# Kernel tuning notes

Hardware: AMD Instinct MI355X
Metric: run time of the kernel (lower is better)

The kernel has to match this reference:

```python
import jax, jax.numpy as jnp
import numpy as np

SPATIAL_SCALE = 0.0625
GAMMA = 0.1  # mmcv DeformRoIPool default
NUM_HEADS = 1


def deform_roi_pool(features, rois, offsets, spatial_scale=SPATIAL_SCALE, gamma=GAMMA):
    """mmcv-style deformable RoI (align) pooling, sampling_ratio=1.
    features: (B,C,H,W); rois: (N,5)=[b,x1,y1,x2,y2]; offsets: (P,oh,ow,2) (dw,dh).
    Returns (P,N,C,oh,ow)."""
    B, C, H, W = features.shape
    N = rois.shape[0]
    P, oh, ow, _ = offsets.shape
    bidx = rois[:, 0].astype(jnp.int32)
    x1 = rois[:, 1] * spatial_scale - 0.5
    y1 = rois[:, 2] * spatial_scale - 0.5
    rw = rois[:, 3] * spatial_scale - 0.5 - x1
    rh = rois[:, 4] * spatial_scale - 0.5 - y1
    bin_w = rw / ow
    bin_h = rh / oh
    gh = jnp.arange(oh, dtype=features.dtype)
    gw = jnp.arange(ow, dtype=features.dtype)
    # bin-center sample points (sampling_ratio=1), deformed by gamma*roi_size*offset
    y = (y1[:, None, None] + (gh[None, :, None] + 0.5) * bin_h[:, None, None])[None]
    y = y + gamma * rh[None, :, None, None] * offsets[:, None, :, :, 1]  # (P,N,oh,ow)
    x = (x1[:, None, None] + (gw[None, None, :] + 0.5) * bin_w[:, None, None])[None]
    x = x + gamma * rw[None, :, None, None] * offsets[:, None, :, :, 0]
    valid = (y > -1.0) & (y < H) & (x > -1.0) & (x < W)
    yc = jnp.clip(y, 0.0, H - 1)
    xc = jnp.clip(x, 0.0, W - 1)
    y0 = jnp.floor(yc).astype(jnp.int32)
    x0 = jnp.floor(xc).astype(jnp.int32)
    y1i = jnp.minimum(y0 + 1, H - 1)
    x1i = jnp.minimum(x0 + 1, W - 1)
    ly = yc - y0.astype(yc.dtype)
    lx = xc - x0.astype(xc.dtype)
    hy = 1.0 - ly
    hx = 1.0 - lx
    f = features.reshape(B, C, H * W)
    bb = jnp.broadcast_to(bidx[None, :, None, None], (P, N, oh, ow))

    def g(yi, xi):
        return f[bb, :, yi * W + xi]  # (P,N,oh,ow,C)

    val = (g(y0, x0) * (hy * hx)[..., None] + g(y0, x1i) * (hy * lx)[..., None]
           + g(y1i, x0) * (ly * hx)[..., None] + g(y1i, x1i) * (ly * lx)[..., None])
    val = jnp.where(valid[..., None], val, 0.0)
    return jnp.transpose(val, (0, 1, 4, 2, 3))  # (P,N,C,oh,ow)


def setup_inputs() -> dict:
    key = jax.random.key(0)
    ks = jax.random.split(key, 9)
    B, C, Hf, Wf = 4, 256, 128, 128
    N, oh, ow, P = 512, 7, 7, 4
    features = jax.random.normal(ks[0], (B, C, Hf, Wf), jnp.float32)
    bidx = jax.random.randint(ks[1], (N,), 0, B).astype(jnp.float32)
    xy1 = jax.random.uniform(ks[2], (N, 2), jnp.float32, 0.0, 1700.0)
    wh = jax.random.uniform(ks[3], (N, 2), jnp.float32, 32.0, 300.0)
    rois = jnp.concatenate([bidx[:, None], xy1, xy1 + wh], axis=1)  # (N,5)
    per_point_offsets = jax.random.normal(ks[4], (P, oh, ow, 2), jnp.float32) * 0.001
    queries = jax.random.normal(ks[5], (oh * ow, C), jnp.float32) * 0.02
    w_proj = jax.random.normal(ks[6], (C, C), jnp.float32) * 0.02
    b_proj = jnp.zeros((C,), jnp.float32)
    in_proj_w = jax.random.normal(ks[7], (3 * C, C), jnp.float32) * 0.02
    in_proj_b = jnp.zeros((3 * C,), jnp.float32)
    out_proj_w = jax.random.normal(ks[8], (C, C), jnp.float32) * 0.02
    out_proj_b = jnp.zeros((C,), jnp.float32)
    return dict(features=features, rois=rois, per_point_offsets=per_point_offsets,
                queries=queries, w_proj=w_proj, b_proj=b_proj,
                in_proj_w=in_proj_w, in_proj_b=in_proj_b,
                out_proj_w=out_proj_w, out_proj_b=out_proj_b)


def reference(features, rois, per_point_offsets, queries, w_proj, b_proj,
              in_proj_w, in_proj_b, out_proj_w, out_proj_b):
    samples = deform_roi_pool(features, rois, per_point_offsets)  # (P,N,C,oh,ow)
    P, N, C, oh, ow = samples.shape
    # 1x1 conv projection
    proj = jnp.einsum('pnchw,dc->pndhw', samples, w_proj) + b_proj[None, None, :, None, None]
    kv = jnp.transpose(proj, (0, 1, 3, 4, 2)).reshape(P, N * oh * ow, C)  # (P,B,C)
    q = jnp.tile(queries, (N, 1))  # (B,C), B=(n,h,w) order
    Wq, Wk, Wv = in_proj_w[:C], in_proj_w[C:2 * C], in_proj_w[2 * C:]
    bq, bk, bv = in_proj_b[:C], in_proj_b[C:2 * C], in_proj_b[2 * C:]
    H = NUM_HEADS
    d = C // H
    Q = (q @ Wq.T + bq).reshape(-1, H, d)
    K = (kv @ Wk.T + bk).reshape(P, -1, H, d)
    V = (kv @ Wv.T + bv).reshape(P, -1, H, d)
    scores = jnp.einsum('bhd,pbhd->bhp', Q, K) * (d ** -0.5)
    attn = jax.nn.softmax(scores, axis=-1)  # over the P sampled points
    out = jnp.einsum('bhp,pbhd->bhd', attn, V).reshape(-1, C)
    out = out @ out_proj_w.T + out_proj_b
    return out.reshape(N, oh, ow, C).transpose(0, 3, 1, 2)  # (N,C,oh,ow)
```

## Files before the change

kernel.cpp:

```cpp
#include <hip/hip_runtime.h>
#include <math.h>

#define C_DIM 256
#define H_DIM 128
#define W_DIM 128
#define B_DIM 4
#define HW (H_DIM*W_DIM)
#define N_ROIS 512
#define OH 7
#define OW 7
#define TOKENS (N_ROIS*OH*OW)
#define SPS 0.0625f
#define GAMMA 0.1f
#define SCALE 0.0625f

typedef __attribute__((ext_vector_type(8))) short bf16x8;
typedef __attribute__((ext_vector_type(4))) float f32x4;
typedef __attribute__((ext_vector_type(4))) unsigned short us4;

__device__ inline unsigned short f2bf_rne(float f) {
    unsigned int b = __float_as_uint(f);
    b += 0x7fffu + ((b >> 16) & 1u);
    return (unsigned short)(b >> 16);
}

__global__ void precompute1(const float* __restrict__ w_proj,
                            const float* __restrict__ in_proj_w,
                            const float* __restrict__ in_proj_b,
                            const float* __restrict__ queries,
                            const float* __restrict__ b_proj,
                            float* __restrict__ A_k, float* __restrict__ A_v,
                            float* __restrict__ Qhat, float* __restrict__ cv) {
    int idx = blockIdx.x * 256 + threadIdx.x;
    if (idx < 65536) {
        int i = idx >> 8, j = idx & 255;
        const float* wk = in_proj_w + (size_t)(256 + i) * 256;
        float s = 0.f;
        for (int t = 0; t < 256; t++) s += wk[t] * w_proj[t * 256 + j];
        A_k[idx] = s;
    } else if (idx < 131072) {
        int e = idx - 65536;
        int i = e >> 8, j = e & 255;
        const float* wv = in_proj_w + (size_t)(512 + i) * 256;
        float s = 0.f;
        for (int t = 0; t < 256; t++) s += wv[t] * w_proj[t * 256 + j];
        A_v[e] = s;
    } else if (idx < 143616) {
        int e = idx - 131072;
        int s_ = e >> 8, i = e & 255;
        const float* q  = queries + (size_t)s_ * 256;
        const float* wq = in_proj_w + (size_t)i * 256;
        float s = in_proj_b[i];
        for (int t = 0; t < 256; t++) s += q[t] * wq[t];
        Qhat[e] = s;
    } else {
        int i = idx - 143616;
        const float* wv = in_proj_w + (size_t)(512 + i) * 256;
        float s = in_proj_b[512 + i];
        for (int t = 0; t < 256; t++) s += wv[t] * b_proj[t];
        cv[i] = s;
    }
}

__global__ void precompute2(const float* __restrict__ Qhat,
                            const float* __restrict__ A_k,
                            const float* __restrict__ A_v,
                            const float* __restrict__ out_proj_w,
                            const float* __restrict__ out_proj_b,
                            const float* __restrict__ cv,
                            float* __restrict__ u,
                            unsigned short* __restrict__ Mh,
                            unsigned short* __restrict__ Ml,
                            float* __restrict__ Mtp, int writeMtp,
                            float* __restrict__ c_out) {
    int idx = blockIdx.x * 256 + threadIdx.x;
    if (idx < 12544) {
        int s_ = idx >> 8, j = idx & 255;
        const float* qh = Qhat + (size_t)s_ * 256;
        float s = 0.f;
        for (int i = 0; i < 256; i++) s += qh[i] * A_k[i * 256 + j];
        u[idx] = s;
    } else if (idx < 78080) {
        int e = idx - 12544;
        int c = e >> 8, d = e & 255;
        const float* wo = out_proj_w + (size_t)c * 256;
        float s = 0.f;
        for (int i = 0; i < 256; i++) s += wo[i] * A_v[i * 256 + d];
        unsigned short hi = f2bf_rne(s);
        float fh = __uint_as_float(((unsigned int)hi) << 16);
        unsigned short lo = f2bf_rne(s - fh);
        Mh[(size_t)c * 256 + d] = hi;
        Ml[(size_t)c * 256 + d] = lo;
        if (writeMtp)
            Mtp[((size_t)(d >> 2) * 256 + c) * 4 + (d & 3)] = s;
    } else {
        int c = idx - 78080;
        const float* wo = out_proj_w + (size_t)c * 256;
        float s = out_proj_b[c];
        for (int i = 0; i < 256; i++) s += wo[i] * cv[i];
        c_out[c] = s;
    }
}

__global__ void transpose_nchw_nhwc(const float* __restrict__ f,
                                    float* __restrict__ ft) {
    __shared__ float tile[64][65];
    int b  = blockIdx.z;
    int c0 = blockIdx.y * 64;
    int s0 = blockIdx.x * 64;
    const float* fin = f + (size_t)b * C_DIM * HW;
    int sl = threadIdx.x & 63, cw = threadIdx.x >> 6;
    #pragma unroll
    for (int k = 0; k < 16; k++) {
        int cl = cw + k * 4;
        tile[cl][sl] = fin[(size_t)(c0 + cl) * HW + s0 + sl];
    }
    __syncthreads();
    float* fo = ft + (size_t)b * HW * C_DIM;
    int cl = threadIdx.x & 63, sw = threadIdx.x >> 6;
    #pragma unroll
    for (int k = 0; k < 16; k++) {
        int sl2 = sw + k * 4;
        fo[(size_t)(s0 + sl2) * C_DIM + c0 + cl] = tile[cl][sl2];
    }
}

__global__ void sample_nhwc(const float* __restrict__ feat_t,
                            const float* __restrict__ rois,
                            const float* __restrict__ offs,
                            const float* __restrict__ u,
                            float* __restrict__ m_out) {
    int wave = threadIdx.x >> 6;
    int lane = threadIdx.x & 63;
    int token = blockIdx.x * 4 + wave;
    int n = token / 49;
    int t = token - n * 49;
    int h = t / 7;
    int w = t - h * 7;

    const float* r = rois + (size_t)n * 5;
    int bi   = (int)r[0];
    float x1 = r[1] * SPS - 0.5f;
    float y1 = r[2] * SPS - 0.5f;
    float rw = r[3] * SPS - 0.5f - x1;
    float rh = r[4] * SPS - 0.5f - y1;
    float bw = rw * (1.0f / 7.0f);
    float bh = rh * (1.0f / 7.0f);

    const float* fb = feat_t + (size_t)bi * HW * C_DIM;
    int c4 = lane * 4;
    float4 uv = *(const float4*)(u + (size_t)t * 256 + c4);

    float4 sv[4];
    float  part[4];
    #pragma unroll
    for (int p = 0; p < 4; p++) {
        float offw = offs[((p * 7 + h) * 7 + w) * 2 + 0];
        float offh = offs[((p * 7 + h) * 7 + w) * 2 + 1];
        float y = y1 + ((float)h + 0.5f) * bh + GAMMA * rh * offh;
        float x = x1 + ((float)w + 0.5f) * bw + GAMMA * rw * offw;
        bool valid = (y > -1.0f) && (y < (float)H_DIM) && (x > -1.0f) && (x < (float)W_DIM);
        float yc = fminf(fmaxf(y, 0.f), 127.f);
        float xc = fminf(fmaxf(x, 0.f), 127.f);
        int y0i = (int)floorf(yc);
        int x0i = (int)floorf(xc);
        int y1i = min(y0i + 1, 127);
        int x1i = min(x0i + 1, 127);
        float ly = yc - (float)y0i, lx = xc - (float)x0i;
        float hy = 1.f - ly, hx = 1.f - lx;
        float4 v00 = *(const float4*)(fb + (size_t)(y0i * W_DIM + x0i) * C_DIM + c4);
        float4 v01 = *(const float4*)(fb + (size_t)(y0i * W_DIM + x1i) * C_DIM + c4);
        float4 v10 = *(const float4*)(fb + (size_t)(y1i * W_DIM + x0i) * C_DIM + c4);
        float4 v11 = *(const float4*)(fb + (size_t)(y1i * W_DIM + x1i) * C_DIM + c4);
        float w00 = hy * hx, w01 = hy * lx, w10 = ly * hx, w11 = ly * lx;
        float4 v;
        v.x = w00 * v00.x + w01 * v01.x + w10 * v10.x + w11 * v11.x;
        v.y = w00 * v00.y + w01 * v01.y + w10 * v10.y + w11 * v11.y;
        v.z = w00 * v00.z + w01 * v01.z + w10 * v10.z + w11 * v11.z;
        v.w = w00 * v00.w + w01 * v01.w + w10 * v10.w + w11 * v11.w;
        if (!valid) { v.x = 0.f; v.y = 0.f; v.z = 0.f; v.w = 0.f; }
        sv[p] = v;
        part[p] = uv.x * v.x + uv.y * v.y + uv.z * v.z + uv.w * v.w;
    }
    #pragma unroll
    for (int mbit = 1; mbit < 64; mbit <<= 1) {
        #pragma unroll
        for (int p = 0; p < 4; p++) part[p] += __shfl_xor(part[p], mbit, 64);
    }
    float sc0 = part[0] * SCALE, sc1 = part[1] * SCALE;
    float sc2 = part[2] * SCALE, sc3 = part[3] * SCALE;
    float mx = fmaxf(fmaxf(sc0, sc1), fmaxf(sc2, sc3));
    float e0 = __expf(sc0 - mx), e1 = __expf(sc1 - mx);
    float e2 = __expf(sc2 - mx), e3 = __expf(sc3 - mx);
    float inv = 1.f / (e0 + e1 + e2 + e3);
    float4 m;
    m.x = (e0 * sv[0].x + e1 * sv[1].x + e2 * sv[2].x + e3 * sv[3].x) * inv;
    m.y = (e0 * sv[0].y + e1 * sv[1].y + e2 * sv[2].y + e3 * sv[3].y) * inv;
    m.z = (e0 * sv[0].z + e1 * sv[1].z + e2 * sv[2].z + e3 * sv[3].z) * inv;
    m.w = (e0 * sv[0].w + e1 * sv[1].w + e2 * sv[2].w + e3 * sv[3].w) * inv;
    *(float4*)(m_out + (size_t)token * 256 + c4) = m;
}

__global__ void sample_generic(const float* __restrict__ feat,
                               const float* __restrict__ rois,
                               const float* __restrict__ offs,
                               const float* __restrict__ u,
                               float* __restrict__ m_out,
                               int ch_stride, int pix_stride) {
    __shared__ float red[4][4];
    int token = blockIdx.x;
    int n = token / 49;
    int t = token - n * 49;
    int h = t / 7;
    int w = t - h * 7;
    const float* r = rois + (size_t)n * 5;
    int bi   = (int)r[0];
    float x1 = r[1] * SPS - 0.5f;
    float y1 = r[2] * SPS - 0.5f;
    float rw = r[3] * SPS - 0.5f - x1;
    float rh = r[4] * SPS - 0.5f - y1;
    float bw = rw * (1.0f / 7.0f);
    float bh = rh * (1.0f / 7.0f);
    int c = threadIdx.x;
    const float* fb = feat + (size_t)bi * HW * C_DIM;
    float u_c = u[(size_t)t * 256 + c];
    float sv[4], part[4];
    #pragma unroll
    for (int p = 0; p < 4; p++) {
        float offw = offs[((p * 7 + h) * 7 + w) * 2 + 0];
        float offh = offs[((p * 7 + h) * 7 + w) * 2 + 1];
        float y = y1 + ((float)h + 0.5f) * bh + GAMMA * rh * offh;
        float x = x1 + ((float)w + 0.5f) * bw + GAMMA * rw * offw;
        bool valid = (y > -1.0f) && (y < (float)H_DIM) && (x > -1.0f) && (x < (float)W_DIM);
        float yc = fminf(fmaxf(y, 0.f), 127.f);
        float xc = fminf(fmaxf(x, 0.f), 127.f);
        int y0i = (int)floorf(yc);
        int x0i = (int)floorf(xc);
        int y1i = min(y0i + 1, 127);
        int x1i = min(x0i + 1, 127);
        float ly = yc - (float)y0i, lx = xc - (float)x0i;
        float hy = 1.f - ly, hx = 1.f - lx;
        float v00 = fb[(size_t)(y0i * W_DIM + x0i) * pix_stride + (size_t)c * ch_stride];
        float v01 = fb[(size_t)(y0i * W_DIM + x1i) * pix_stride + (size_t)c * ch_stride];
        float v10 = fb[(size_t)(y1i * W_DIM + x0i) * pix_stride + (size_t)c * ch_stride];
        float v11 = fb[(size_t)(y1i * W_DIM + x1i) * pix_stride + (size_t)c * ch_stride];
        float v = hy * hx * v00 + hy * lx * v01 + ly * hx * v10 + ly * lx * v11;
        v = valid ? v : 0.f;
        sv[p] = v;
        part[p] = u_c * v;
    }
    #pragma unroll
    for (int o = 32; o >= 1; o >>= 1) {
        #pragma unroll
        for (int p = 0; p < 4; p++) part[p] += __shfl_down(part[p], o, 64);
    }
    int wv = threadIdx.x >> 6, lane = threadIdx.x & 63;
    if (lane == 0) {
        red[wv][0] = part[0]; red[wv][1] = part[1];
        red[wv][2] = part[2]; red[wv][3] = part[3];
    }
    __syncthreads();
    float sc0 = (red[0][0] + red[1][0] + red[2][0] + red[3][0]) * SCALE;
    float sc1 = (red[0][1] + red[1][1] + red[2][1] + red[3][1]) * SCALE;
    float sc2 = (red[0][2] + red[1][2] + red[2][2] + red[3][2]) * SCALE;
    float sc3 = (red[0][3] + red[1][3] + red[2][3] + red[3][3]) * SCALE;
    float mx = fmaxf(fmaxf(sc0, sc1), fmaxf(sc2, sc3));
    float e0 = __expf(sc0 - mx), e1 = __expf(sc1 - mx);
    float e2 = __expf(sc2 - mx), e3 = __expf(sc3 - mx);
    float inv = 1.f / (e0 + e1 + e2 + e3);
    m_out[(size_t)token * 256 + c] =
        (e0 * sv[0] + e1 * sv[1] + e2 * sv[2] + e3 * sv[3]) * inv;
}

__global__ void __launch_bounds__(256) roi_gemm_mfma(
        const float* m,
        const unsigned short* __restrict__ Mh,
        const unsigned short* __restrict__ Ml,
        const float* __restrict__ c_out,
        float* out) {
    __shared__ __align__(16) unsigned short lds[32768];
    unsigned short* Ah = lds;
    unsigned short* Al = lds + 64 * 256;

    int tid = threadIdx.x;
    int n = blockIdx.x;
    const float* mb = m + (size_t)n * 12544;

    for (int i = tid; i < 3136; i += 256) {
        float4 f = *(const float4*)(mb + (size_t)i * 4);
        us4 hi, lo;
        unsigned short h;
        h = f2bf_rne(f.x); hi.x = h; lo.x = f2bf_rne(f.x - __uint_as_float(((unsigned int)h) << 16));
        h = f2bf_rne(f.y); hi.y = h; lo.y = f2bf_rne(f.y - __uint_as_float(((unsigned int)h) << 16));
        h = f2bf_rne(f.z); hi.z = h; lo.z = f2bf_rne(f.z - __uint_as_float(((unsigned int)h) << 16));
        h = f2bf_rne(f.w); hi.w = h; lo.w = f2bf_rne(f.w - __uint_as_float(((unsigned int)h) << 16));
        int t = i >> 6;
        int d = (i & 63) * 4;
        *(us4*)(Ah + t * 256 + d) = hi;
        *(us4*)(Al + t * 256 + d) = lo;
    }
    __syncthreads();

    int lane = tid & 63;
    int wave = tid >> 6;
    int col  = lane & 15;
    int quad = lane >> 4;
    int c_base = wave * 64;

    f32x4 zero = {0.f, 0.f, 0.f, 0.f};
    f32x4 acc[4][4];
    #pragma unroll
    for (int i = 0; i < 4; i++)
        #pragma unroll
        for (int j = 0; j < 4; j++) acc[i][j] = zero;

    for (int ks = 0; ks < 8; ks++) {
        bf16x8 afh[4], afl[4];
        #pragma unroll
        for (int rt = 0; rt < 4; rt++) {
            int row = rt * 16 + col;
            int off = row * 256 + ks * 32 + quad * 8;
            afh[rt] = *(const bf16x8*)(Ah + off);
            afl[rt] = *(const bf16x8*)(Al + off);
        }
        #pragma unroll
        for (int ct = 0; ct < 4; ct++) {
            size_t boff = (size_t)(c_base + ct * 16 + col) * 256 + ks * 32 + quad * 8;
            bf16x8 bfh = *(const bf16x8*)(Mh + boff);
            bf16x8 bfl = *(const bf16x8*)(Ml + boff);
            #pragma unroll
            for (int rt = 0; rt < 4; rt++) {
                acc[rt][ct] = __builtin_amdgcn_mfma_f32_16x16x32_bf16(afh[rt], bfh, acc[rt][ct], 0, 0, 0);
                acc[rt][ct] = __builtin_amdgcn_mfma_f32_16x16x32_bf16(afl[rt], bfh, acc[rt][ct], 0, 0, 0);
                acc[rt][ct] = __builtin_amdgcn_mfma_f32_16x16x32_bf16(afh[rt], bfl, acc[rt][ct], 0, 0, 0);
            }
        }
    }

    __syncthreads();
    float* ostage = (float*)lds;
    #pragma unroll
    for (int rt = 0; rt < 4; rt++) {
        #pragma unroll
        for (int ct = 0; ct < 4; ct++) {
            int c = c_base + ct * 16 + col;
            float bias = c_out[c];
            #pragma unroll
            for (int r = 0; r < 4; r++) {
                int t = rt * 16 + quad * 4 + r;
                if (t < 49) ostage[c * 53 + t] = acc[rt][ct][r] + bias;
            }
        }
    }
    __syncthreads();
    float* ob = out + (size_t)n * 12544;
    for (int k = 0; k < 49; k++) {
        int flat = k * 256 + tid;
        int c2 = flat / 49;
        int t2 = flat - c2 * 49;
        ob[flat] = ostage[c2 * 53 + t2];
    }
}

__global__ void __launch_bounds__(256) roi_gemm(const float* __restrict__ m,
                                                const float* __restrict__ Mtp,
                                                const float* __restrict__ c_out,
                                                float* __restrict__ out) {
    __shared__ float mlds[49 * 260];
    int c = threadIdx.x;
    int n = blockIdx.x;
    const float* mb = m + (size_t)n * 12544;
    for (int t = 0; t < 49; t++) mlds[t * 260 + c] = mb[t * 256 + c];
    __syncthreads();
    float acc[49];
    #pragma unroll
    for (int t = 0; t < 49; t++) acc[t] = 0.f;
    const float4* Mp = (const float4*)Mtp;
    for (int d4 = 0; d4 < 64; d4++) {
        float4 w4 = Mp[(size_t)d4 * 256 + c];
        #pragma unroll
        for (int t = 0; t < 49; t++) {
            float4 mv = *(const float4*)&mlds[t * 260 + d4 * 4];
            acc[t] = fmaf(w4.x, mv.x, acc[t]);
            acc[t] = fmaf(w4.y, mv.y, acc[t]);
            acc[t] = fmaf(w4.z, mv.z, acc[t]);
            acc[t] = fmaf(w4.w, mv.w, acc[t]);
        }
    }
    float bias = c_out[c];
    __syncthreads();
    #pragma unroll
    for (int t = 0; t < 49; t++) mlds[t * 260 + c] = acc[t] + bias;
    __syncthreads();
    float* ob = out + (size_t)n * 12544;
    for (int k = 0; k < 49; k++) {
        int flat = k * 256 + c;
        int c2 = flat / 49;
        int t2 = flat - c2 * 49;
        ob[flat] = mlds[t2 * 260 + c2];
    }
}

extern "C" void kernel_launch(void* const* d_in, const int* in_sizes, int n_in,
                              void* d_out, int out_size, void* d_ws, size_t ws_size,
                              hipStream_t stream) {
    (void)in_sizes; (void)n_in; (void)out_size;
    const float* features   = (const float*)d_in[0];
    const float* rois       = (const float*)d_in[1];
    const float* offs       = (const float*)d_in[2];
    const float* queries    = (const float*)d_in[3];
    const float* w_proj     = (const float*)d_in[4];
    const float* b_proj     = (const float*)d_in[5];
    const float* in_proj_w  = (const float*)d_in[6];
    const float* in_proj_b  = (const float*)d_in[7];
    const float* out_proj_w = (const float*)d_in[8];
    const float* out_proj_b = (const float*)d_in[9];
    float* out = (float*)d_out;
    float* ws  = (float*)d_ws;

    float* A_k   = ws;
    float* A_v   = A_k  + 65536;
    float* Qhat  = A_v  + 65536;
    float* cv    = Qhat + 12544;
    float* u     = cv   + 256;
    float* c_out = u    + 12544;
    unsigned short* Mh = (unsigned short*)(ws + 156672);
    unsigned short* Ml = (unsigned short*)(ws + 189440);
    float* feat_t = ws + 222208;
    float* Mtp    = ws + 222208;

    size_t needT = ((size_t)222208 + (size_t)16777216) * 4;
    bool useT = ws_size >= needT;

    precompute1<<<562, 256, 0, stream>>>(w_proj, in_proj_w, in_proj_b,
                                         queries, b_proj, A_k, A_v, Qhat, cv);
    precompute2<<<306, 256, 0, stream>>>(Qhat, A_k, A_v, out_proj_w, out_proj_b,
                                         cv, u, Mh, Ml, Mtp, useT ? 0 : 1, c_out);

    float* m = out;
    if (useT) {
        transpose_nchw_nhwc<<<dim3(256, 4, 4), 256, 0, stream>>>(features, feat_t);
        sample_nhwc<<<TOKENS / 4, 256, 0, stream>>>(feat_t, rois, offs, u, m);
        roi_gemm_mfma<<<512, 256, 0, stream>>>(m, Mh, Ml, c_out, out);
    } else {
        sample_generic<<<TOKENS, 256, 0, stream>>>(features, rois, offs, u, m, HW, 1);
        roi_gemm<<<512, 256, 0, stream>>>(m, Mtp, c_out, out);
    }
}
```

Before: 203.2 us.

## Fuse sampling and MFMA GEMM per RoI with bf16 NHWC features

The NHWC transpose now writes bf16 instead of fp32, which halves the feature-map footprint that the gathers read. The sampling/softmax stage and the MFMA projection GEMM are merged into one kernel per RoI. The attention-weighted samples are kept in LDS as bf16, so the fp32 intermediate round-trip through global memory and a separate launch go away. The GEMM drops the lo-part of the activation split (two MFMAs instead of three per tile), which lowers precision of both the sampled features and the GEMM input. The fallback path also gains a separate workspace buffer for the intermediate.

```diff
diff --git a/kernel.cpp b/kernel.cpp
--- a/kernel.cpp
+++ b/kernel.cpp
@@ -17,11 +17,15 @@
 typedef __attribute__((ext_vector_type(8))) short bf16x8;
 typedef __attribute__((ext_vector_type(4))) float f32x4;
 typedef __attribute__((ext_vector_type(4))) unsigned short us4;
+typedef __attribute__((ext_vector_type(8))) unsigned short us8;
 
 __device__ inline unsigned short f2bf_rne(float f) {
     unsigned int b = __float_as_uint(f);
     b += 0x7fffu + ((b >> 16) & 1u);
     return (unsigned short)(b >> 16);
+}
+__device__ inline float bfu(unsigned short u) {
+    return __uint_as_float(((unsigned int)u) << 16);
 }
 
 __global__ void precompute1(const float* __restrict__ w_proj,
@@ -87,7 +91,7 @@
         float s = 0.f;
         for (int i = 0; i < 256; i++) s += wo[i] * A_v[i * 256 + d];
         unsigned short hi = f2bf_rne(s);
-        float fh = __uint_as_float(((unsigned int)hi) << 16);
+        float fh = bfu(hi);
         unsigned short lo = f2bf_rne(s - fh);
         Mh[(size_t)c * 256 + d] = hi;
         Ml[(size_t)c * 256 + d] = lo;
@@ -102,8 +106,8 @@
     }
 }
 
-__global__ void transpose_nchw_nhwc(const float* __restrict__ f,
-                                    float* __restrict__ ft) {
+__global__ void transpose_bf16(const float* __restrict__ f,
+                               unsigned short* __restrict__ ft) {
     __shared__ float tile[64][65];
     int b  = blockIdx.z;
     int c0 = blockIdx.y * 64;
@@ -116,89 +120,164 @@
         tile[cl][sl] = fin[(size_t)(c0 + cl) * HW + s0 + sl];
     }
     __syncthreads();
-    float* fo = ft + (size_t)b * HW * C_DIM;
+    unsigned short* fo = ft + (size_t)b * HW * C_DIM;
     int cl = threadIdx.x & 63, sw = threadIdx.x >> 6;
     #pragma unroll
     for (int k = 0; k < 16; k++) {
         int sl2 = sw + k * 4;
-        fo[(size_t)(s0 + sl2) * C_DIM + c0 + cl] = tile[cl][sl2];
-    }
-}
-
-__global__ void sample_nhwc(const float* __restrict__ feat_t,
-                            const float* __restrict__ rois,
-                            const float* __restrict__ offs,
-                            const float* __restrict__ u,
-                            float* __restrict__ m_out) {
-    int wave = threadIdx.x >> 6;
-    int lane = threadIdx.x & 63;
-    int token = blockIdx.x * 4 + wave;
-    int n = token / 49;
-    int t = token - n * 49;
-    int h = t / 7;
-    int w = t - h * 7;
+        fo[(size_t)(s0 + sl2) * C_DIM + c0 + cl] = f2bf_rne(tile[cl][sl2]);
+    }
+}
+
+__global__ void __launch_bounds__(256) fused_sample_gemm(
+        const unsigned short* __restrict__ feat_b,
+        const float* __restrict__ rois,
+        const float* __restrict__ offs,
+        const float* __restrict__ u,
+        const unsigned short* __restrict__ Mh,
+        const unsigned short* __restrict__ Ml,
+        const float* __restrict__ c_out,
+        float* __restrict__ out) {
+    __shared__ __align__(16) char ldsraw[54272];
+    unsigned short* A = (unsigned short*)ldsraw;
+
+    int tid = threadIdx.x;
+    int n = blockIdx.x;
 
     const float* r = rois + (size_t)n * 5;
     int bi   = (int)r[0];
     float x1 = r[1] * SPS - 0.5f;
-    float y1 = r[2] * SPS - 0.5f;
+    float y1v = r[2] * SPS - 0.5f;
     float rw = r[3] * SPS - 0.5f - x1;
-    float rh = r[4] * SPS - 0.5f - y1;
+    float rh = r[4] * SPS - 0.5f - y1v;
     float bw = rw * (1.0f / 7.0f);
     float bh = rh * (1.0f / 7.0f);
-
-    const float* fb = feat_t + (size_t)bi * HW * C_DIM;
-    int c4 = lane * 4;
-    float4 uv = *(const float4*)(u + (size_t)t * 256 + c4);
-
-    float4 sv[4];
-    float  part[4];
-    #pragma unroll
-    for (int p = 0; p < 4; p++) {
-        float offw = offs[((p * 7 + h) * 7 + w) * 2 + 0];
-        float offh = offs[((p * 7 + h) * 7 + w) * 2 + 1];
-        float y = y1 + ((float)h + 0.5f) * bh + GAMMA * rh * offh;
-        float x = x1 + ((float)w + 0.5f) * bw + GAMMA * rw * offw;
-        bool valid = (y > -1.0f) && (y < (float)H_DIM) && (x > -1.0f) && (x < (float)W_DIM);
-        float yc = fminf(fmaxf(y, 0.f), 127.f);
-        float xc = fminf(fmaxf(x, 0.f), 127.f);
-        int y0i = (int)floorf(yc);
-        int x0i = (int)floorf(xc);
-        int y1i = min(y0i + 1, 127);
-        int x1i = min(x0i + 1, 127);
-        float ly = yc - (float)y0i, lx = xc - (float)x0i;
-        float hy = 1.f - ly, hx = 1.f - lx;
-        float4 v00 = *(const float4*)(fb + (size_t)(y0i * W_DIM + x0i) * C_DIM + c4);
-        float4 v01 = *(const float4*)(fb + (size_t)(y0i * W_DIM + x1i) * C_DIM + c4);
-        float4 v10 = *(const float4*)(fb + (size_t)(y1i * W_DIM + x0i) * C_DIM + c4);
-        float4 v11 = *(const float4*)(fb + (size_t)(y1i * W_DIM + x1i) * C_DIM + c4);
-        float w00 = hy * hx, w01 = hy * lx, w10 = ly * hx, w11 = ly * lx;
-        float4 v;
-        v.x = w00 * v00.x + w01 * v01.x + w10 * v10.x + w11 * v11.x;
-        v.y = w00 * v00.y + w01 * v01.y + w10 * v10.y + w11 * v11.y;
-        v.z = w00 * v00.z + w01 * v01.z + w10 * v10.z + w11 * v11.z;
-        v.w = w00 * v00.w + w01 * v01.w + w10 * v10.w + w11 * v11.w;
-        if (!valid) { v.x = 0.f; v.y = 0.f; v.z = 0.f; v.w = 0.f; }
-        sv[p] = v;
-        part[p] = uv.x * v.x + uv.y * v.y + uv.z * v.z + uv.w * v.w;
-    }
-    #pragma unroll
-    for (int mbit = 1; mbit < 64; mbit <<= 1) {
-        #pragma unroll
-        for (int p = 0; p < 4; p++) part[p] += __shfl_xor(part[p], mbit, 64);
-    }
-    float sc0 = part[0] * SCALE, sc1 = part[1] * SCALE;
-    float sc2 = part[2] * SCALE, sc3 = part[3] * SCALE;
-    float mx = fmaxf(fmaxf(sc0, sc1), fmaxf(sc2, sc3));
-    float e0 = __expf(sc0 - mx), e1 = __expf(sc1 - mx);
-    float e2 = __expf(sc2 - mx), e3 = __expf(sc3 - mx);
-    float inv = 1.f / (e0 + e1 + e2 + e3);
-    float4 m;
-    m.x = (e0 * sv[0].x + e1 * sv[1].x + e2 * sv[2].x + e3 * sv[3].x) * inv;
-    m.y = (e0 * sv[0].y + e1 * sv[1].y + e2 * sv[2].y + e3 * sv[3].y) * inv;
-    m.z = (e0 * sv[0].z + e1 * sv[1].z + e2 * sv[2].z + e3 * sv[3].z) * inv;
-    m.w = (e0 * sv[0].w + e1 * sv[1].w + e2 * sv[2].w + e3 * sv[3].w) * inv;
-    *(float4*)(m_out + (size_t)token * 256 + c4) = m;
+    const unsigned short* fb = feat_b + (size_t)bi * HW * C_DIM;
+
+    int lane32 = tid & 31;
+    int halfw  = tid >> 5;
+    int c8 = lane32 * 8;
+
+    for (int t = halfw; t < 49; t += 8) {
+        int hb = t / 7, wb = t - hb * 7;
+        const float* up = u + (size_t)t * 256 + c8;
+        float uu[8];
+        *(float4*)uu       = *(const float4*)up;
+        *(float4*)(uu + 4) = *(const float4*)(up + 4);
+
+        float sv[4][8];
+        float part[4];
+        #pragma unroll
+        for (int p = 0; p < 4; p++) {
+            float offw = offs[((p * 7 + hb) * 7 + wb) * 2 + 0];
+            float offh = offs[((p * 7 + hb) * 7 + wb) * 2 + 1];
+            float y = y1v + ((float)hb + 0.5f) * bh + GAMMA * rh * offh;
+            float x = x1  + ((float)wb + 0.5f) * bw + GAMMA * rw * offw;
+            bool valid = (y > -1.0f) && (y < 128.0f) && (x > -1.0f) && (x < 128.0f);
+            float yc = fminf(fmaxf(y, 0.f), 127.f);
+            float xc = fminf(fmaxf(x, 0.f), 127.f);
+            int y0i = (int)yc, x0i = (int)xc;
+            int y1i = min(y0i + 1, 127), x1i = min(x0i + 1, 127);
+            float ly = yc - (float)y0i, lx = xc - (float)x0i;
+            float hy = 1.f - ly, hx = 1.f - lx;
+            float w00 = hy * hx, w01 = hy * lx, w10 = ly * hx, w11 = ly * lx;
+            if (!valid) { w00 = 0.f; w01 = 0.f; w10 = 0.f; w11 = 0.f; }
+            us8 r00 = *(const us8*)(fb + (size_t)(y0i * W_DIM + x0i) * C_DIM + c8);
+            us8 r01 = *(const us8*)(fb + (size_t)(y0i * W_DIM + x1i) * C_DIM + c8);
+            us8 r10 = *(const us8*)(fb + (size_t)(y1i * W_DIM + x0i) * C_DIM + c8);
+            us8 r11 = *(const us8*)(fb + (size_t)(y1i * W_DIM + x1i) * C_DIM + c8);
+            float accp = 0.f;
+            #pragma unroll
+            for (int j = 0; j < 8; j++) {
+                float v = w00 * bfu(r00[j]) + w01 * bfu(r01[j])
+                        + w10 * bfu(r10[j]) + w11 * bfu(r11[j]);
+                sv[p][j] = v;
+                accp = fmaf(uu[j], v, accp);
+            }
+            part[p] = accp;
+        }
+        #pragma unroll
+        for (int mk = 1; mk <= 16; mk <<= 1) {
+            #pragma unroll
+            for (int p = 0; p < 4; p++) part[p] += __shfl_xor(part[p], mk, 64);
+        }
+        float sc0 = part[0] * SCALE, sc1 = part[1] * SCALE;
+        float sc2 = part[2] * SCALE, sc3 = part[3] * SCALE;
+        float mx = fmaxf(fmaxf(sc0, sc1), fmaxf(sc2, sc3));
+        float e0 = __expf(sc0 - mx), e1 = __expf(sc1 - mx);
+        float e2 = __expf(sc2 - mx), e3 = __expf(sc3 - mx);
+        float inv = 1.f / (e0 + e1 + e2 + e3);
+        us8 o8;
+        #pragma unroll
+        for (int j = 0; j < 8; j++) {
+            float mv = (e0 * sv[0][j] + e1 * sv[1][j]
+                      + e2 * sv[2][j] + e3 * sv[3][j]) * inv;
+            o8[j] = f2bf_rne(mv);
+        }
+        *(us8*)(A + t * 264 + c8) = o8;
+    }
+    for (int i = tid; i < 480; i += 256) {
+        int row = 49 + (i >> 5);
+        int cs = (i & 31) * 8;
+        us8 z = {0, 0, 0, 0, 0, 0, 0, 0};
+        *(us8*)(A + row * 264 + cs) = z;
+    }
+    __syncthreads();
+
+    int lane = tid & 63;
+    int wave = tid >> 6;
+    int col  = lane & 15;
+    int quad = lane >> 4;
+    int cbase = wave * 64;
+
+    f32x4 zero = {0.f, 0.f, 0.f, 0.f};
+    f32x4 acc[4][4];
+    #pragma unroll
+    for (int i = 0; i < 4; i++)
+        #pragma unroll
+        for (int j = 0; j < 4; j++) acc[i][j] = zero;
+
+    for (int ks = 0; ks < 8; ks++) {
+        bf16x8 af[4];
+        #pragma unroll
+        for (int rt = 0; rt < 4; rt++)
+            af[rt] = *(const bf16x8*)(A + (rt * 16 + col) * 264 + ks * 32 + quad * 8);
+        #pragma unroll
+        for (int ct = 0; ct < 4; ct++) {
+            size_t bo = (size_t)(cbase + ct * 16 + col) * 256 + ks * 32 + quad * 8;
+            bf16x8 bh8 = *(const bf16x8*)(Mh + bo);
+            bf16x8 bl8 = *(const bf16x8*)(Ml + bo);
+            #pragma unroll
+            for (int rt = 0; rt < 4; rt++) {
+                acc[rt][ct] = __builtin_amdgcn_mfma_f32_16x16x32_bf16(af[rt], bh8, acc[rt][ct], 0, 0, 0);
+                acc[rt][ct] = __builtin_amdgcn_mfma_f32_16x16x32_bf16(af[rt], bl8, acc[rt][ct], 0, 0, 0);
+            }
+        }
+    }
+
+    __syncthreads();
+    float* ostage = (float*)ldsraw;
+    #pragma unroll
+    for (int rt = 0; rt < 4; rt++) {
+        #pragma unroll
+        for (int ct = 0; ct < 4; ct++) {
+            int c = cbase + ct * 16 + col;
+            float bias = c_out[c];
+            #pragma unroll
+            for (int rr = 0; rr < 4; rr++) {
+                int t = rt * 16 + quad * 4 + rr;
+                if (t < 49) ostage[c * 53 + t] = acc[rt][ct][rr] + bias;
+            }
+        }
+    }
+    __syncthreads();
+    float* ob = out + (size_t)n * 12544;
+    for (int k = 0; k < 49; k++) {
+        int flat = k * 256 + tid;
+        int c2 = flat / 49;
+        int t2 = flat - c2 * 49;
+        ob[flat] = ostage[c2 * 53 + t2];
+    }
 }
 
 __global__ void sample_generic(const float* __restrict__ feat,
@@ -272,96 +351,6 @@
         (e0 * sv[0] + e1 * sv[1] + e2 * sv[2] + e3 * sv[3]) * inv;
 }
 
-__global__ void __launch_bounds__(256) roi_gemm_mfma(
-        const float* m,
-        const unsigned short* __restrict__ Mh,
-        const unsigned short* __restrict__ Ml,
-        const float* __restrict__ c_out,
-        float* out) {
-    __shared__ __align__(16) unsigned short lds[32768];
-    unsigned short* Ah = lds;
-    unsigned short* Al = lds + 64 * 256;
-
-    int tid = threadIdx.x;
-    int n = blockIdx.x;
-    const float* mb = m + (size_t)n * 12544;
-
-    for (int i = tid; i < 3136; i += 256) {
-        float4 f = *(const float4*)(mb + (size_t)i * 4);
-        us4 hi, lo;
-        unsigned short h;
-        h = f2bf_rne(f.x); hi.x = h; lo.x = f2bf_rne(f.x - __uint_as_float(((unsigned int)h) << 16));
-        h = f2bf_rne(f.y); hi.y = h; lo.y = f2bf_rne(f.y - __uint_as_float(((unsigned int)h) << 16));
-        h = f2bf_rne(f.z); hi.z = h; lo.z = f2bf_rne(f.z - __uint_as_float(((unsigned int)h) << 16));
-        h = f2bf_rne(f.w); hi.w = h; lo.w = f2bf_rne(f.w - __uint_as_float(((unsigned int)h) << 16));
-        int t = i >> 6;
-        int d = (i & 63) * 4;
-        *(us4*)(Ah + t * 256 + d) = hi;
-        *(us4*)(Al + t * 256 + d) = lo;
-    }
-    __syncthreads();
-
-    int lane = tid & 63;
-    int wave = tid >> 6;
-    int col  = lane & 15;
-    int quad = lane >> 4;
-    int c_base = wave * 64;
-
-    f32x4 zero = {0.f, 0.f, 0.f, 0.f};
-    f32x4 acc[4][4];
-    #pragma unroll
-    for (int i = 0; i < 4; i++)
-        #pragma unroll
-        for (int j = 0; j < 4; j++) acc[i][j] = zero;
-
-    for (int ks = 0; ks < 8; ks++) {
-        bf16x8 afh[4], afl[4];
-        #pragma unroll
-        for (int rt = 0; rt < 4; rt++) {
-            int row = rt * 16 + col;
-            int off = row * 256 + ks * 32 + quad * 8;
-            afh[rt] = *(const bf16x8*)(Ah + off);
-            afl[rt] = *(const bf16x8*)(Al + off);
-        }
-        #pragma unroll
-        for (int ct = 0; ct < 4; ct++) {
-            size_t boff = (size_t)(c_base + ct * 16 + col) * 256 + ks * 32 + quad * 8;
-            bf16x8 bfh = *(const bf16x8*)(Mh + boff);
-            bf16x8 bfl = *(const bf16x8*)(Ml + boff);
-            #pragma unroll
-            for (int rt = 0; rt < 4; rt++) {
-                acc[rt][ct] = __builtin_amdgcn_mfma_f32_16x16x32_bf16(afh[rt], bfh, acc[rt][ct], 0, 0, 0);
-                acc[rt][ct] = __builtin_amdgcn_mfma_f32_16x16x32_bf16(afl[rt], bfh, acc[rt][ct], 0, 0, 0);
-                acc[rt][ct] = __builtin_amdgcn_mfma_f32_16x16x32_bf16(afh[rt], bfl, acc[rt][ct], 0, 0, 0);
-            }
-        }
-    }
-
-    __syncthreads();
-    float* ostage = (float*)lds;
-    #pragma unroll
-    for (int rt = 0; rt < 4; rt++) {
-        #pragma unroll
-        for (int ct = 0; ct < 4; ct++) {
-            int c = c_base + ct * 16 + col;
-            float bias = c_out[c];
-            #pragma unroll
-            for (int r = 0; r < 4; r++) {
-                int t = rt * 16 + quad * 4 + r;
-                if (t < 49) ostage[c * 53 + t] = acc[rt][ct][r] + bias;
-            }
-        }
-    }
-    __syncthreads();
-    float* ob = out + (size_t)n * 12544;
-    for (int k = 0; k < 49; k++) {
-        int flat = k * 256 + tid;
-        int c2 = flat / 49;
-        int t2 = flat - c2 * 49;
-        ob[flat] = ostage[c2 * 53 + t2];
-    }
-}
-
 __global__ void __launch_bounds__(256) roi_gemm(const float* __restrict__ m,
                                                 const float* __restrict__ Mtp,
                                                 const float* __restrict__ c_out,
@@ -426,10 +415,12 @@
     float* c_out = u    + 12544;
     unsigned short* Mh = (unsigned short*)(ws + 156672);
     unsigned short* Ml = (unsigned short*)(ws + 189440);
-    float* feat_t = ws + 222208;
+    unsigned short* feat_b = (unsigned short*)(ws + 222208);
     float* Mtp    = ws + 222208;
-
-    size_t needT = ((size_t)222208 + (size_t)16777216) * 4;
+    float* m_fb   = ws + 222208 + 65536;
+
+    size_t needT = ((size_t)222208 + (size_t)8388608) * 4;
+    size_t needF = ((size_t)222208 + (size_t)65536 + (size_t)TOKENS * 256) * 4;
     bool useT = ws_size >= needT;
 
     precompute1<<<562, 256, 0, stream>>>(w_proj, in_proj_w, in_proj_b,
@@ -437,12 +428,12 @@
     precompute2<<<306, 256, 0, stream>>>(Qhat, A_k, A_v, out_proj_w, out_proj_b,
                                          cv, u, Mh, Ml, Mtp, useT ? 0 : 1, c_out);
 
-    float* m = out;
     if (useT) {
-        transpose_nchw_nhwc<<<dim3(256, 4, 4), 256, 0, stream>>>(features, feat_t);
-        sample_nhwc<<<TOKENS / 4, 256, 0, stream>>>(feat_t, rois, offs, u, m);
-        roi_gemm_mfma<<<512, 256, 0, stream>>>(m, Mh, Ml, c_out, out);
+        transpose_bf16<<<dim3(256, 4, 4), 256, 0, stream>>>(features, feat_b);
+        fused_sample_gemm<<<N_ROIS, 256, 0, stream>>>(feat_b, rois, offs, u,
+                                                      Mh, Ml, c_out, out);
     } else {
+        float* m = (ws_size >= needF) ? m_fb : out;
         sample_generic<<<TOKENS, 256, 0, stream>>>(features, rois, offs, u, m, HW, 1);
         roi_gemm<<<512, 256, 0, stream>>>(m, Mtp, c_out, out);
     }
```

New measurement: 180.8 us. -11.0%, faster.
